# Kernel tuning notes

Measured on AMD Instinct MI355X. Metric: run time of the kernel, lower is better.

The kernel has to match this reference:

```python
import jax, jax.numpy as jnp
import numpy as np

B, W, K = 8, 200, 100   # batch, window_size, n_features
KS = 7                   # conv kernel size
HID = 150                # GRU hidden dim
ALPHA = 0.2              # leaky relu slope
FE = 2 * W               # feature GAT embed dim (gatv2 doubles window_size)
TE = 2 * K               # temporal GAT embed dim (gatv2 doubles n_features)


def setup_inputs() -> dict:
    key = jax.random.key(0)
    ks = jax.random.split(key, 16)
    s = lambda k, shape, sc=0.05: jax.random.normal(k, shape, jnp.float32) * sc
    return {
        "x": jax.random.normal(ks[0], (B, W, K), jnp.float32),
        "conv_w": s(ks[1], (K, K, KS)),
        "conv_b": s(ks[2], (K,)),
        "f_lin_w": s(ks[3], (2 * W, FE)),
        "f_lin_b": s(ks[4], (FE,)),
        "f_a": s(ks[5], (FE,)),
        "f_bias": s(ks[6], (K, K)),
        "t_lin_w": s(ks[7], (2 * K, TE)),
        "t_lin_b": s(ks[8], (TE,)),
        "t_a": s(ks[9], (TE,)),
        "t_bias": s(ks[10], (W, W)),
        "w_ih": s(ks[11], (3 * HID, 3 * K)),
        "w_hh": s(ks[12], (3 * HID, HID)),
        "b_ih": s(ks[13], (3 * HID,)),
        "b_hh": s(ks[14], (3 * HID,)),
    }


def _leaky(x):
    return jnp.where(x >= 0, x, ALPHA * x)


def _gatv2(v, lin_w, lin_b, a, bias):
    """GATv2 layer over fully-connected graph. v: (b, N, D).
    e_ij = a . leakyrelu(W [v_i || v_j] + b_lin); out = sigmoid(softmax(e+bias) @ v).
    Splitting W rows avoids materializing the (b,N,N,2D) concat tensor."""
    D = v.shape[-1]
    w1, w2 = lin_w[:D], lin_w[D:]
    si = jnp.einsum('bnd,de->bne', v, w1)  # contribution of node i (repeated)
    sj = jnp.einsum('bnd,de->bne', v, w2)  # contribution of node j (alternating)
    g = _leaky(si[:, :, None, :] + sj[:, None, :, :] + lin_b)  # (b,N,N,E)
    e = jnp.einsum('bije,e->bij', g, a) + bias                 # (b,N,N)
    attn = jax.nn.softmax(e, axis=2)
    return jax.nn.sigmoid(jnp.einsum('bij,bjd->bid', attn, v))  # (b,N,D)


def _forward(x, conv_w, conv_b, f_lin_w, f_lin_b, f_a, f_bias,
             t_lin_w, t_lin_b, t_a, t_bias, w_ih, w_hh, b_ih, b_hh):
    # ConvLayer: permute to (b,K,W), pad 3 both sides, conv1d k=7, relu, permute back
    xc = jnp.transpose(x, (0, 2, 1))
    xc = jax.lax.conv_general_dilated(xc, conv_w, (1,), [((KS - 1) // 2, (KS - 1) // 2)],
                                      dimension_numbers=('NCH', 'OIH', 'NCH'))
    xc = jax.nn.relu(xc + conv_b[None, :, None])
    xc = jnp.transpose(xc, (0, 2, 1))  # (b, W, K)

    # Feature GAT: nodes = features, per-node vector = window
    h_feat = _gatv2(jnp.transpose(xc, (0, 2, 1)), f_lin_w, f_lin_b, f_a, f_bias)
    h_feat = jnp.transpose(h_feat, (0, 2, 1))  # (b, W, K)
    # Temporal GAT: nodes = timesteps, per-node vector = features
    h_temp = _gatv2(xc, t_lin_w, t_lin_b, t_a, t_bias)  # (b, W, K)

    h_cat = jnp.concatenate([xc, h_feat, h_temp], axis=2)  # (b, W, 3K)

    # Single-layer GRU, torch gate order (r, z, n), batch_first; return final hidden
    def step(h, xt):
        gi = xt @ w_ih.T + b_ih
        gh = h @ w_hh.T + b_hh
        ir, iz, inn = jnp.split(gi, 3, axis=-1)
        hr, hz, hn = jnp.split(gh, 3, axis=-1)
        r = jax.nn.sigmoid(ir + hr)
        z = jax.nn.sigmoid(iz + hz)
        n = jnp.tanh(inn + r * hn)
        return (1.0 - z) * n + z * h, None

    h0 = jnp.zeros((x.shape[0], HID), x.dtype)
    h_end, _ = jax.lax.scan(step, h0, jnp.transpose(h_cat, (1, 0, 2)))
    return h_end  # (b, HID)


def reference(x, conv_w, conv_b, f_lin_w, f_lin_b, f_a, f_bias,
              t_lin_w, t_lin_b, t_a, t_bias, w_ih, w_hh, b_ih, b_hh):
    return _forward(x, conv_w, conv_b, f_lin_w, f_lin_b, f_a, f_bias,
                    t_lin_w, t_lin_b, t_a, t_bias, w_ih, w_hh, b_ih, b_hh)
```

## Files before the change

### kernel.cpp

```cpp
#include <hip/hip_runtime.h>
#include <math.h>

#define NB   8
#define NW   200
#define NK   100
#define KSZ  7
#define NHID 150
#define NFE  400
#define NTE  200
#define NG   450
#define NCIN 300
#define ALPHAC 0.2f

typedef __attribute__((ext_vector_type(8))) short bf8;
typedef __attribute__((ext_vector_type(4))) float f32x4;

__device__ __forceinline__ float sigmoidf_(float x){
  return 1.0f/(1.0f + __expf(-x));
}
__device__ __forceinline__ float tanhf_(float x){
  float xc = fminf(fmaxf(x, -15.f), 15.f);
  float e = __expf(2.f*xc);
  return (e - 1.f)/(e + 1.f);
}
__device__ __forceinline__ unsigned short f2bf(float f){
  unsigned int u = __float_as_uint(f);
  unsigned int r = u + 0x7FFFu + ((u>>16)&1u);
  return (unsigned short)(r>>16);
}

__global__ void prep_kernel(const float* conv_w, const float* w_ih, const float* w_hh,
                            float* conv_wT, float* w_ihT, unsigned int* Bfrag){
  int idx = blockIdx.x*256 + threadIdx.x;
  const int n1 = NK*NK*KSZ;
  const int n2 = NG*NCIN;
  const int n3 = 32*5*64*4;
  if (idx < n1){
    int k = idx % NK; int it = idx / NK;
    int i = it / KSZ, t = it % KSZ;
    conv_wT[idx] = conv_w[(k*NK + i)*KSZ + t];
  } else if (idx < n1 + n2){
    int o = idx - n1; int g = o % NG; int c = o / NG;
    w_ihT[o] = w_ih[g*NCIN + c];
  } else if (idx < n1 + n2 + n3){
    int o = idx - n1 - n2;
    int n   = o / 1280;
    int rem = o % 1280;
    int ks  = rem / 256;
    int rem2= rem % 256;
    int l   = rem2 >> 2;
    int d   = rem2 & 3;
    int col = n*16 + (l & 15);
    int k0  = ks*32 + (l >> 4)*8 + d*2;
    unsigned short lo = 0, hi = 0;
    if (col < NG){
      if (k0     < NHID) lo = f2bf(w_hh[col*NHID + k0]);
      if (k0 + 1 < NHID) hi = f2bf(w_hh[col*NHID + k0 + 1]);
    }
    Bfrag[o] = ((unsigned int)hi << 16) | lo;
  }
}

__global__ void conv_kernel(const float* x, const float* conv_b, const float* conv_wT, float* xc){
  int idx = blockIdx.x*256 + threadIdx.x;
  if (idx >= NB*NW*NK) return;
  int k = idx % NK; int w = (idx/NK) % NW; int b = idx/(NK*NW);
  float acc = conv_b[k];
  const float* xb = x + b*NW*NK;
  for (int t = 0; t < KSZ; ++t){
    int ws = w + t - 3;
    if (ws < 0 || ws >= NW) continue;
    const float* xr = xb + ws*NK;
    const float* wr = conv_wT + t*NK + k;
    #pragma unroll 4
    for (int i = 0; i < NK; ++i){
      acc += xr[i] * wr[i*KSZ*NK];
    }
  }
  xc[idx] = fmaxf(acc, 0.0f);
}

__global__ void fgat_sisj(const float* xc, const float* f_lin_w, float* si, float* sj){
  __shared__ __align__(16) float vt[NW*4];
  int b = blockIdx.x / 25; int n0 = (blockIdx.x % 25)*4;
  int tid = threadIdx.x;
  for (int idx = tid; idx < NW*4; idx += 512){
    int d = idx >> 2, nn = idx & 3;
    vt[idx] = xc[(b*NW + d)*NK + n0 + nn];
  }
  __syncthreads();
  if (tid >= NFE) return;
  int e = tid;
  float a1[4] = {0,0,0,0}, a2[4] = {0,0,0,0};
  for (int d = 0; d < NW; ++d){
    float w1 = f_lin_w[d*NFE + e];
    float w2 = f_lin_w[(NW + d)*NFE + e];
    float4 v = *(const float4*)&vt[d*4];
    a1[0] += v.x*w1; a1[1] += v.y*w1; a1[2] += v.z*w1; a1[3] += v.w*w1;
    a2[0] += v.x*w2; a2[1] += v.y*w2; a2[2] += v.z*w2; a2[3] += v.w*w2;
  }
  #pragma unroll
  for (int nn = 0; nn < 4; ++nn){
    si[(b*NK + n0+nn)*NFE + e] = a1[nn];
    sj[(b*NK + n0+nn)*NFE + e] = a2[nn];
  }
}

__global__ void tgat_sisj(const float* xc, const float* t_lin_w, float* si, float* sj){
  __shared__ __align__(16) float vt[NK*4];
  int b = blockIdx.x / 50; int n0 = (blockIdx.x % 50)*4;
  int tid = threadIdx.x;
  for (int idx = tid; idx < NK*4; idx += 256){
    int d = idx >> 2, nn = idx & 3;
    vt[idx] = xc[(b*NW + n0+nn)*NK + d];
  }
  __syncthreads();
  if (tid >= NTE) return;
  int e = tid;
  float a1[4] = {0,0,0,0}, a2[4] = {0,0,0,0};
  for (int d = 0; d < NK; ++d){
    float w1 = t_lin_w[d*NTE + e];
    float w2 = t_lin_w[(NK + d)*NTE + e];
    float4 v = *(const float4*)&vt[d*4];
    a1[0] += v.x*w1; a1[1] += v.y*w1; a1[2] += v.z*w1; a1[3] += v.w*w1;
    a2[0] += v.x*w2; a2[1] += v.y*w2; a2[2] += v.z*w2; a2[3] += v.w*w2;
  }
  #pragma unroll
  for (int nn = 0; nn < 4; ++nn){
    si[(b*NW + n0+nn)*NTE + e] = a1[nn];
    sj[(b*NW + n0+nn)*NTE + e] = a2[nn];
  }
}

__global__ void fgat_attn(const float* xc, const float* si, const float* sj,
                          const float* f_lin_b, const float* f_a, const float* f_bias,
                          float* h_featT){
  __shared__ float sib[NFE], av[NFE], attn[NK], red[128];
  int b = blockIdx.x / NK, i = blockIdx.x % NK;
  int tid = threadIdx.x;
  for (int e = tid; e < NFE; e += 128){
    sib[e] = si[(b*NK + i)*NFE + e] + f_lin_b[e];
    av[e]  = f_a[e];
  }
  __syncthreads();
  float ej = -1e30f;
  if (tid < NK){
    const float* sjr = sj + (b*NK + tid)*NFE;
    float acc = 0.f;
    for (int e = 0; e < NFE; ++e){
      float tv = sib[e] + sjr[e];
      float lk = fmaxf(tv, 0.f) + ALPHAC*fminf(tv, 0.f);
      acc += av[e]*lk;
    }
    ej = acc + f_bias[i*NK + tid];
  }
  red[tid] = ej; __syncthreads();
  for (int s = 64; s > 0; s >>= 1){ if (tid < s) red[tid] = fmaxf(red[tid], red[tid+s]); __syncthreads(); }
  float m = red[0]; __syncthreads();
  float ex = (tid < NK) ? __expf(ej - m) : 0.f;
  red[tid] = ex; __syncthreads();
  for (int s = 64; s > 0; s >>= 1){ if (tid < s) red[tid] += red[tid+s]; __syncthreads(); }
  float denom = red[0];
  if (tid < NK) attn[tid] = ex / denom;
  __syncthreads();
  for (int d = tid; d < NW; d += 128){
    const float* xr = xc + (b*NW + d)*NK;
    float acc = 0.f;
    for (int j = 0; j < NK; ++j) acc += attn[j]*xr[j];
    h_featT[(b*NW + d)*NK + i] = sigmoidf_(acc);
  }
}

__global__ void tgat_attn(const float* xc, const float* si, const float* sj,
                          const float* t_lin_b, const float* t_a, const float* t_bias,
                          float* h_temp){
  __shared__ float sib[NTE], av[NTE], attn[NW], red[256];
  int b = blockIdx.x / NW, i = blockIdx.x % NW;
  int tid = threadIdx.x;
  for (int e = tid; e < NTE; e += 256){
    sib[e] = si[(b*NW + i)*NTE + e] + t_lin_b[e];
    av[e]  = t_a[e];
  }
  __syncthreads();
  float ej = -1e30f;
  if (tid < NW){
    const float* sjr = sj + (b*NW + tid)*NTE;
    float acc = 0.f;
    for (int e = 0; e < NTE; ++e){
      float tv = sib[e] + sjr[e];
      float lk = fmaxf(tv, 0.f) + ALPHAC*fminf(tv, 0.f);
      acc += av[e]*lk;
    }
    ej = acc + t_bias[i*NW + tid];
  }
  red[tid] = ej; __syncthreads();
  for (int s = 128; s > 0; s >>= 1){ if (tid < s) red[tid] = fmaxf(red[tid], red[tid+s]); __syncthreads(); }
  float m = red[0]; __syncthreads();
  float ex = (tid < NW) ? __expf(ej - m) : 0.f;
  red[tid] = ex; __syncthreads();
  for (int s = 128; s > 0; s >>= 1){ if (tid < s) red[tid] += red[tid+s]; __syncthreads(); }
  float denom = red[0];
  if (tid < NW) attn[tid] = ex / denom;
  __syncthreads();
  for (int d = tid; d < NK; d += 256){
    float acc = 0.f;
    for (int j = 0; j < NW; ++j) acc += attn[j]*xc[(b*NW + j)*NK + d];
    h_temp[(b*NW + i)*NK + d] = sigmoidf_(acc);
  }
}

__global__ void gi_kernel(const float* xc, const float* h_featT, const float* h_temp,
                          const float* w_ihT, const float* b_ih, float* gi){
  __shared__ __align__(16) float hc[NCIN*8];
  int b = blockIdx.x / 25; int t0 = (blockIdx.x % 25)*8;
  int tid = threadIdx.x;
  for (int idx = tid; idx < NCIN*8; idx += 512){
    int tt = idx / NCIN; int c = idx % NCIN;
    int base = (b*NW + t0 + tt)*NK;
    float v;
    if (c < NK)        v = xc[base + c];
    else if (c < 2*NK) v = h_featT[base + c - NK];
    else               v = h_temp[base + c - 2*NK];
    hc[c*8 + tt] = v;
  }
  __syncthreads();
  if (tid >= NG) return;
  int g = tid;
  float bi = b_ih[g];
  float acc[8];
  #pragma unroll
  for (int tt = 0; tt < 8; ++tt) acc[tt] = bi;
  for (int c = 0; c < NCIN; ++c){
    float wv = w_ihT[c*NG + g];
    float4 h0 = *(const float4*)&hc[c*8];
    float4 h1 = *(const float4*)&hc[c*8+4];
    acc[0] += h0.x*wv; acc[1] += h0.y*wv; acc[2] += h0.z*wv; acc[3] += h0.w*wv;
    acc[4] += h1.x*wv; acc[5] += h1.y*wv; acc[6] += h1.z*wv; acc[7] += h1.w*wv;
  }
  #pragma unroll
  for (int tt = 0; tt < 8; ++tt)
    gi[((t0+tt)*NB + b)*NG + g] = acc[tt];
}

#define STASH(B0,B1,B2,B3, FR) { \
  int4 wq = Bq[(FR)*64 + lane]; \
  asm volatile("v_accvgpr_write_b32 " B0 ", %0\n\t" \
               "v_accvgpr_write_b32 " B1 ", %1\n\t" \
               "v_accvgpr_write_b32 " B2 ", %2\n\t" \
               "v_accvgpr_write_b32 " B3 ", %3" \
               :: "v"(wq.x), "v"(wq.y), "v"(wq.z), "v"(wq.w) \
               : B0, B1, B2, B3); }
#define MMA_INIT(ACC, AF, BR, C0,C1,C2,C3) \
  asm volatile("v_mfma_f32_16x16x32_bf16 %0, %1, " BR ", 0" \
               : "=v"(ACC) : "v"(AF) : C0,C1,C2,C3);
#define MMA_ACC(ACC, AF, BR, C0,C1,C2,C3) \
  asm volatile("v_mfma_f32_16x16x32_bf16 %0, %1, " BR ", %0" \
               : "+v"(ACC) : "v"(AF) : C0,C1,C2,C3);

__global__ void __launch_bounds__(512, 2) gru_kernel(const float* gi, const int4* Bq,
                                                     const float* b_hh, float* out){
  __shared__ __align__(16) unsigned short h_bf[16*176];
  __shared__ __align__(16) float h_f32[8*152];
  __shared__ __align__(16) float gh[16*516];
  int tid = threadIdx.x;
  int lane = tid & 63;
  int wv = tid >> 6;
  int agrp = lane >> 4;
  int arow = lane & 15;
  int crow = agrp*4;
  int ccol = arow;

  int p0 = tid, p1 = tid + 512, p2 = tid + 1024;
  int b0 = p0/NHID, u0 = p0%NHID;
  int b1 = p1/NHID, u1 = p1%NHID;
  bool v2 = (p2 < NB*NHID);
  int b2 = v2 ? p2/NHID : 0, u2 = v2 ? p2%NHID : 0;
  float bhr0 = b_hh[u0], bhz0 = b_hh[NHID+u0], bhn0 = b_hh[2*NHID+u0];
  float bhr1 = b_hh[u1], bhz1 = b_hh[NHID+u1], bhn1 = b_hh[2*NHID+u1];
  float bhr2 = b_hh[u2], bhz2 = b_hh[NHID+u2], bhn2 = b_hh[2*NHID+u2];

  STASH("a0","a1","a2","a3",     (wv)*5+0)
  STASH("a4","a5","a6","a7",     (wv)*5+1)
  STASH("a8","a9","a10","a11",   (wv)*5+2)
  STASH("a12","a13","a14","a15", (wv)*5+3)
  STASH("a16","a17","a18","a19", (wv)*5+4)
  STASH("a20","a21","a22","a23", (wv+8)*5+0)
  STASH("a24","a25","a26","a27", (wv+8)*5+1)
  STASH("a28","a29","a30","a31", (wv+8)*5+2)
  STASH("a32","a33","a34","a35", (wv+8)*5+3)
  STASH("a36","a37","a38","a39", (wv+8)*5+4)
  STASH("a40","a41","a42","a43", (wv+16)*5+0)
  STASH("a44","a45","a46","a47", (wv+16)*5+1)
  STASH("a48","a49","a50","a51", (wv+16)*5+2)
  STASH("a52","a53","a54","a55", (wv+16)*5+3)
  STASH("a56","a57","a58","a59", (wv+16)*5+4)
  STASH("a60","a61","a62","a63", (wv+24)*5+0)
  STASH("a64","a65","a66","a67", (wv+24)*5+1)
  STASH("a68","a69","a70","a71", (wv+24)*5+2)
  STASH("a72","a73","a74","a75", (wv+24)*5+3)
  STASH("a76","a77","a78","a79", (wv+24)*5+4)

  for (int i = tid; i < 16*176; i += 512) h_bf[i] = 0;
  for (int i = tid; i < 8*152;  i += 512) h_f32[i] = 0.f;
  __syncthreads();

  const bf8* HB = (const bf8*)h_bf;
  int abase = arow*22 + agrp;

  for (int t = 0; t < NW; ++t){
    const float* gt = gi + t*NB*NG;
    float gr0 = gt[b0*NG+u0], gz0 = gt[b0*NG+NHID+u0], gn0 = gt[b0*NG+2*NHID+u0];
    float gr1 = gt[b1*NG+u1], gz1 = gt[b1*NG+NHID+u1], gn1 = gt[b1*NG+2*NHID+u1];
    float gr2 = 0.f, gz2 = 0.f, gn2 = 0.f;
    if (v2){ gr2 = gt[b2*NG+u2]; gz2 = gt[b2*NG+NHID+u2]; gn2 = gt[b2*NG+2*NHID+u2]; }

    bf8 A0 = HB[abase],    A1 = HB[abase+4],  A2 = HB[abase+8],
        A3 = HB[abase+12], A4 = HB[abase+16];

    f32x4 c0, c1, c2, c3;
    MMA_INIT(c0, A0, "a[0:3]",   "a0","a1","a2","a3")
    MMA_INIT(c1, A0, "a[20:23]", "a20","a21","a22","a23")
    MMA_INIT(c2, A0, "a[40:43]", "a40","a41","a42","a43")
    MMA_INIT(c3, A0, "a[60:63]", "a60","a61","a62","a63")
    MMA_ACC (c0, A1, "a[4:7]",   "a4","a5","a6","a7")
    MMA_ACC (c1, A1, "a[24:27]", "a24","a25","a26","a27")
    MMA_ACC (c2, A1, "a[44:47]", "a44","a45","a46","a47")
    MMA_ACC (c3, A1, "a[64:67]", "a64","a65","a66","a67")
    MMA_ACC (c0, A2, "a[8:11]",  "a8","a9","a10","a11")
    MMA_ACC (c1, A2, "a[28:31]", "a28","a29","a30","a31")
    MMA_ACC (c2, A2, "a[48:51]", "a48","a49","a50","a51")
    MMA_ACC (c3, A2, "a[68:71]", "a68","a69","a70","a71")
    MMA_ACC (c0, A3, "a[12:15]", "a12","a13","a14","a15")
    MMA_ACC (c1, A3, "a[32:35]", "a32","a33","a34","a35")
    MMA_ACC (c2, A3, "a[52:55]", "a52","a53","a54","a55")
    MMA_ACC (c3, A3, "a[72:75]", "a72","a73","a74","a75")
    MMA_ACC (c0, A4, "a[16:19]", "a16","a17","a18","a19")
    MMA_ACC (c1, A4, "a[36:39]", "a36","a37","a38","a39")
    MMA_ACC (c2, A4, "a[56:59]", "a56","a57","a58","a59")
    MMA_ACC (c3, A4, "a[76:79]", "a76","a77","a78","a79")
    asm volatile("s_nop 7\n\ts_nop 7" ::: );

    {
      float* g0 = &gh[crow*516 + (wv   )*16 + ccol];
      float* g1 = &gh[crow*516 + (wv+ 8)*16 + ccol];
      float* g2 = &gh[crow*516 + (wv+16)*16 + ccol];
      float* g3 = &gh[crow*516 + (wv+24)*16 + ccol];
      g0[0]=c0[0]; g0[516]=c0[1]; g0[1032]=c0[2]; g0[1548]=c0[3];
      g1[0]=c1[0]; g1[516]=c1[1]; g1[1032]=c1[2]; g1[1548]=c1[3];
      g2[0]=c2[0]; g2[516]=c2[1]; g2[1032]=c2[2]; g2[1548]=c2[3];
      g3[0]=c3[0]; g3[516]=c3[1]; g3[1032]=c3[2]; g3[1548]=c3[3];
    }
    __syncthreads();

    {
      float r = sigmoidf_(gr0 + gh[b0*516+u0]        + gh[(8+b0)*516+u0]        + bhr0);
      float z = sigmoidf_(gz0 + gh[b0*516+NHID+u0]   + gh[(8+b0)*516+NHID+u0]   + bhz0);
      float n = tanhf_  (gn0 + r*(gh[b0*516+2*NHID+u0] + gh[(8+b0)*516+2*NHID+u0] + bhn0));
      float hold = h_f32[b0*152+u0];
      float hn = (1.f - z)*n + z*hold;
      h_f32[b0*152+u0] = hn;
      unsigned int ub = __float_as_uint(hn);
      unsigned int hi = (ub + 0x7FFFu + ((ub>>16)&1u)) >> 16;
      h_bf[b0*176+u0] = (unsigned short)hi;
      float lo = hn - __uint_as_float(hi<<16);
      unsigned int ul = __float_as_uint(lo);
      h_bf[(8+b0)*176+u0] = (unsigned short)((ul + 0x7FFFu + ((ul>>16)&1u)) >> 16);
    }
    {
      float r = sigmoidf_(gr1 + gh[b1*516+u1]        + gh[(8+b1)*516+u1]        + bhr1);
      float z = sigmoidf_(gz1 + gh[b1*516+NHID+u1]   + gh[(8+b1)*516+NHID+u1]   + bhz1);
      float n = tanhf_  (gn1 + r*(gh[b1*516+2*NHID+u1] + gh[(8+b1)*516+2*NHID+u1] + bhn1));
      float hold = h_f32[b1*152+u1];
      float hn = (1.f - z)*n + z*hold;
      h_f32[b1*152+u1] = hn;
      unsigned int ub = __float_as_uint(hn);
      unsigned int hi = (ub + 0x7FFFu + ((ub>>16)&1u)) >> 16;
      h_bf[b1*176+u1] = (unsigned short)hi;
      float lo = hn - __uint_as_float(hi<<16);
      unsigned int ul = __float_as_uint(lo);
      h_bf[(8+b1)*176+u1] = (unsigned short)((ul + 0x7FFFu + ((ul>>16)&1u)) >> 16);
    }
    if (v2){
      float r = sigmoidf_(gr2 + gh[b2*516+u2]        + gh[(8+b2)*516+u2]        + bhr2);
      float z = sigmoidf_(gz2 + gh[b2*516+NHID+u2]   + gh[(8+b2)*516+NHID+u2]   + bhz2);
      float n = tanhf_  (gn2 + r*(gh[b2*516+2*NHID+u2] + gh[(8+b2)*516+2*NHID+u2] + bhn2));
      float hold = h_f32[b2*152+u2];
      float hn = (1.f - z)*n + z*hold;
      h_f32[b2*152+u2] = hn;
      unsigned int ub = __float_as_uint(hn);
      unsigned int hi = (ub + 0x7FFFu + ((ub>>16)&1u)) >> 16;
      h_bf[b2*176+u2] = (unsigned short)hi;
      float lo = hn - __uint_as_float(hi<<16);
      unsigned int ul = __float_as_uint(lo);
      h_bf[(8+b2)*176+u2] = (unsigned short)((ul + 0x7FFFu + ((ul>>16)&1u)) >> 16);
    }
    __syncthreads();
  }

  out[b0*NHID + u0] = h_f32[b0*152 + u0];
  out[b1*NHID + u1] = h_f32[b1*152 + u1];
  if (v2) out[b2*NHID + u2] = h_f32[b2*152 + u2];
}

extern "C" void kernel_launch(void* const* d_in, const int* in_sizes, int n_in,
                              void* d_out, int out_size, void* d_ws, size_t ws_size,
                              hipStream_t stream){
  const float* x       = (const float*)d_in[0];
  const float* conv_w  = (const float*)d_in[1];
  const float* conv_b  = (const float*)d_in[2];
  const float* f_lin_w = (const float*)d_in[3];
  const float* f_lin_b = (const float*)d_in[4];
  const float* f_a     = (const float*)d_in[5];
  const float* f_bias  = (const float*)d_in[6];
  const float* t_lin_w = (const float*)d_in[7];
  const float* t_lin_b = (const float*)d_in[8];
  const float* t_a     = (const float*)d_in[9];
  const float* t_bias  = (const float*)d_in[10];
  const float* w_ih    = (const float*)d_in[11];
  const float* w_hh    = (const float*)d_in[12];
  const float* b_ih    = (const float*)d_in[13];
  const float* b_hh    = (const float*)d_in[14];

  float* ws      = (float*)d_ws;
  float* xc      = ws;
  float* conv_wT = ws + 160000;
  float* si_f    = ws + 230000;
  float* sj_f    = ws + 550000;
  float* h_featT = ws + 870000;
  float* si_t    = ws + 1030000;
  float* sj_t    = ws + 1350000;
  float* h_temp  = ws + 1670000;
  float* w_ihT   = ws + 1830000;
  float* gi      = ws + 1965000;
  float* BfragF  = ws + 2685000;

  prep_kernel<<<961, 256, 0, stream>>>(conv_w, w_ih, w_hh, conv_wT, w_ihT, (unsigned int*)BfragF);
  conv_kernel<<<(NB*NW*NK + 255)/256, 256, 0, stream>>>(x, conv_b, conv_wT, xc);
  fgat_sisj<<<NB*25, 512, 0, stream>>>(xc, f_lin_w, si_f, sj_f);
  tgat_sisj<<<NB*50, 256, 0, stream>>>(xc, t_lin_w, si_t, sj_t);
  fgat_attn<<<NB*NK, 128, 0, stream>>>(xc, si_f, sj_f, f_lin_b, f_a, f_bias, h_featT);
  tgat_attn<<<NB*NW, 256, 0, stream>>>(xc, si_t, sj_t, t_lin_b, t_a, t_bias, h_temp);
  gi_kernel<<<NB*25, 512, 0, stream>>>(xc, h_featT, h_temp, w_ihT, b_ih, gi);
  gru_kernel<<<1, 512, 0, stream>>>(gi, (const int4*)BfragF, b_hh, (float*)d_out);
}
```

Measured before the change: 434.7 us.

## Run GRU recurrence with 1024 threads, halving MFMA chains per wave

```diff
diff --git a/kernel.cpp b/kernel.cpp
--- a/kernel.cpp
+++ b/kernel.cpp
@@ -257,8 +257,8 @@
   asm volatile("v_mfma_f32_16x16x32_bf16 %0, %1, " BR ", %0" \
                : "+v"(ACC) : "v"(AF) : C0,C1,C2,C3);
 
-__global__ void __launch_bounds__(512, 2) gru_kernel(const float* gi, const int4* Bq,
-                                                     const float* b_hh, float* out){
+__global__ void __launch_bounds__(1024, 4) gru_kernel(const float* gi, const int4* Bq,
+                                                      const float* b_hh, float* out){
   __shared__ __align__(16) unsigned short h_bf[16*176];
   __shared__ __align__(16) float h_f32[8*152];
   __shared__ __align__(16) float gh[16*516];
@@ -270,38 +270,27 @@
   int crow = agrp*4;
   int ccol = arow;
 
-  int p0 = tid, p1 = tid + 512, p2 = tid + 1024;
+  int p0 = tid;
   int b0 = p0/NHID, u0 = p0%NHID;
-  int b1 = p1/NHID, u1 = p1%NHID;
-  bool v2 = (p2 < NB*NHID);
-  int b2 = v2 ? p2/NHID : 0, u2 = v2 ? p2%NHID : 0;
+  bool v1 = (tid < 176);
+  int p1 = tid + 1024;
+  int b1 = v1 ? p1/NHID : 0, u1 = v1 ? p1%NHID : 0;
   float bhr0 = b_hh[u0], bhz0 = b_hh[NHID+u0], bhn0 = b_hh[2*NHID+u0];
   float bhr1 = b_hh[u1], bhz1 = b_hh[NHID+u1], bhn1 = b_hh[2*NHID+u1];
-  float bhr2 = b_hh[u2], bhz2 = b_hh[NHID+u2], bhn2 = b_hh[2*NHID+u2];
 
   STASH("a0","a1","a2","a3",     (wv)*5+0)
   STASH("a4","a5","a6","a7",     (wv)*5+1)
   STASH("a8","a9","a10","a11",   (wv)*5+2)
   STASH("a12","a13","a14","a15", (wv)*5+3)
   STASH("a16","a17","a18","a19", (wv)*5+4)
-  STASH("a20","a21","a22","a23", (wv+8)*5+0)
-  STASH("a24","a25","a26","a27", (wv+8)*5+1)
-  STASH("a28","a29","a30","a31", (wv+8)*5+2)
-  STASH("a32","a33","a34","a35", (wv+8)*5+3)
-  STASH("a36","a37","a38","a39", (wv+8)*5+4)
-  STASH("a40","a41","a42","a43", (wv+16)*5+0)
-  STASH("a44","a45","a46","a47", (wv+16)*5+1)
-  STASH("a48","a49","a50","a51", (wv+16)*5+2)
-  STASH("a52","a53","a54","a55", (wv+16)*5+3)
-  STASH("a56","a57","a58","a59", (wv+16)*5+4)
-  STASH("a60","a61","a62","a63", (wv+24)*5+0)
-  STASH("a64","a65","a66","a67", (wv+24)*5+1)
-  STASH("a68","a69","a70","a71", (wv+24)*5+2)
-  STASH("a72","a73","a74","a75", (wv+24)*5+3)
-  STASH("a76","a77","a78","a79", (wv+24)*5+4)
-
-  for (int i = tid; i < 16*176; i += 512) h_bf[i] = 0;
-  for (int i = tid; i < 8*152;  i += 512) h_f32[i] = 0.f;
+  STASH("a20","a21","a22","a23", (wv+16)*5+0)
+  STASH("a24","a25","a26","a27", (wv+16)*5+1)
+  STASH("a28","a29","a30","a31", (wv+16)*5+2)
+  STASH("a32","a33","a34","a35", (wv+16)*5+3)
+  STASH("a36","a37","a38","a39", (wv+16)*5+4)
+
+  for (int i = tid; i < 16*176; i += 1024) h_bf[i] = 0;
+  for (int i = tid; i < 8*152;  i += 1024) h_f32[i] = 0.f;
   __syncthreads();
 
   const bf8* HB = (const bf8*)h_bf;
@@ -310,45 +299,30 @@
   for (int t = 0; t < NW; ++t){
     const float* gt = gi + t*NB*NG;
     float gr0 = gt[b0*NG+u0], gz0 = gt[b0*NG+NHID+u0], gn0 = gt[b0*NG+2*NHID+u0];
-    float gr1 = gt[b1*NG+u1], gz1 = gt[b1*NG+NHID+u1], gn1 = gt[b1*NG+2*NHID+u1];
-    float gr2 = 0.f, gz2 = 0.f, gn2 = 0.f;
-    if (v2){ gr2 = gt[b2*NG+u2]; gz2 = gt[b2*NG+NHID+u2]; gn2 = gt[b2*NG+2*NHID+u2]; }
+    float gr1 = 0.f, gz1 = 0.f, gn1 = 0.f;
+    if (v1){ gr1 = gt[b1*NG+u1]; gz1 = gt[b1*NG+NHID+u1]; gn1 = gt[b1*NG+2*NHID+u1]; }
 
     bf8 A0 = HB[abase],    A1 = HB[abase+4],  A2 = HB[abase+8],
         A3 = HB[abase+12], A4 = HB[abase+16];
 
-    f32x4 c0, c1, c2, c3;
+    f32x4 c0, c1;
     MMA_INIT(c0, A0, "a[0:3]",   "a0","a1","a2","a3")
     MMA_INIT(c1, A0, "a[20:23]", "a20","a21","a22","a23")
-    MMA_INIT(c2, A0, "a[40:43]", "a40","a41","a42","a43")
-    MMA_INIT(c3, A0, "a[60:63]", "a60","a61","a62","a63")
     MMA_ACC (c0, A1, "a[4:7]",   "a4","a5","a6","a7")
     MMA_ACC (c1, A1, "a[24:27]", "a24","a25","a26","a27")
-    MMA_ACC (c2, A1, "a[44:47]", "a44","a45","a46","a47")
-    MMA_ACC (c3, A1, "a[64:67]", "a64","a65","a66","a67")
     MMA_ACC (c0, A2, "a[8:11]",  "a8","a9","a10","a11")
     MMA_ACC (c1, A2, "a[28:31]", "a28","a29","a30","a31")
-    MMA_ACC (c2, A2, "a[48:51]", "a48","a49","a50","a51")
-    MMA_ACC (c3, A2, "a[68:71]", "a68","a69","a70","a71")
     MMA_ACC (c0, A3, "a[12:15]", "a12","a13","a14","a15")
     MMA_ACC (c1, A3, "a[32:35]", "a32","a33","a34","a35")
-    MMA_ACC (c2, A3, "a[52:55]", "a52","a53","a54","a55")
-    MMA_ACC (c3, A3, "a[72:75]", "a72","a73","a74","a75")
     MMA_ACC (c0, A4, "a[16:19]", "a16","a17","a18","a19")
     MMA_ACC (c1, A4, "a[36:39]", "a36","a37","a38","a39")
-    MMA_ACC (c2, A4, "a[56:59]", "a56","a57","a58","a59")
-    MMA_ACC (c3, A4, "a[76:79]", "a76","a77","a78","a79")
     asm volatile("s_nop 7\n\ts_nop 7" ::: );
 
     {
       float* g0 = &gh[crow*516 + (wv   )*16 + ccol];
-      float* g1 = &gh[crow*516 + (wv+ 8)*16 + ccol];
-      float* g2 = &gh[crow*516 + (wv+16)*16 + ccol];
-      float* g3 = &gh[crow*516 + (wv+24)*16 + ccol];
+      float* g1 = &gh[crow*516 + (wv+16)*16 + ccol];
       g0[0]=c0[0]; g0[516]=c0[1]; g0[1032]=c0[2]; g0[1548]=c0[3];
       g1[0]=c1[0]; g1[516]=c1[1]; g1[1032]=c1[2]; g1[1548]=c1[3];
-      g2[0]=c2[0]; g2[516]=c2[1]; g2[1032]=c2[2]; g2[1548]=c2[3];
-      g3[0]=c3[0]; g3[516]=c3[1]; g3[1032]=c3[2]; g3[1548]=c3[3];
     }
     __syncthreads();
 
@@ -366,7 +340,7 @@
       unsigned int ul = __float_as_uint(lo);
       h_bf[(8+b0)*176+u0] = (unsigned short)((ul + 0x7FFFu + ((ul>>16)&1u)) >> 16);
     }
-    {
+    if (v1){
       float r = sigmoidf_(gr1 + gh[b1*516+u1]        + gh[(8+b1)*516+u1]        + bhr1);
       float z = sigmoidf_(gz1 + gh[b1*516+NHID+u1]   + gh[(8+b1)*516+NHID+u1]   + bhz1);
       float n = tanhf_  (gn1 + r*(gh[b1*516+2*NHID+u1] + gh[(8+b1)*516+2*NHID+u1] + bhn1));
@@ -380,26 +354,11 @@
       unsigned int ul = __float_as_uint(lo);
       h_bf[(8+b1)*176+u1] = (unsigned short)((ul + 0x7FFFu + ((ul>>16)&1u)) >> 16);
     }
-    if (v2){
-      float r = sigmoidf_(gr2 + gh[b2*516+u2]        + gh[(8+b2)*516+u2]        + bhr2);
-      float z = sigmoidf_(gz2 + gh[b2*516+NHID+u2]   + gh[(8+b2)*516+NHID+u2]   + bhz2);
-      float n = tanhf_  (gn2 + r*(gh[b2*516+2*NHID+u2] + gh[(8+b2)*516+2*NHID+u2] + bhn2));
-      float hold = h_f32[b2*152+u2];
-      float hn = (1.f - z)*n + z*hold;
-      h_f32[b2*152+u2] = hn;
-      unsigned int ub = __float_as_uint(hn);
-      unsigned int hi = (ub + 0x7FFFu + ((ub>>16)&1u)) >> 16;
-      h_bf[b2*176+u2] = (unsigned short)hi;
-      float lo = hn - __uint_as_float(hi<<16);
-      unsigned int ul = __float_as_uint(lo);
-      h_bf[(8+b2)*176+u2] = (unsigned short)((ul + 0x7FFFu + ((ul>>16)&1u)) >> 16);
-    }
     __syncthreads();
   }
 
   out[b0*NHID + u0] = h_f32[b0*152 + u0];
-  out[b1*NHID + u1] = h_f32[b1*152 + u1];
-  if (v2) out[b2*NHID + u2] = h_f32[b2*152 + u2];
+  if (v1) out[b1*NHID + u1] = h_f32[b1*152 + u1];
 }
 
 extern "C" void kernel_launch(void* const* d_in, const int* in_sizes, int n_in,
@@ -441,5 +400,5 @@
   fgat_attn<<<NB*NK, 128, 0, stream>>>(xc, si_f, sj_f, f_lin_b, f_a, f_bias, h_featT);
   tgat_attn<<<NB*NW, 256, 0, stream>>>(xc, si_t, sj_t, t_lin_b, t_a, t_bias, h_temp);
   gi_kernel<<<NB*25, 512, 0, stream>>>(xc, h_featT, h_temp, w_ihT, b_ih, gi);
-  gru_kernel<<<1, 512, 0, stream>>>(gi, (const int4*)BfragF, b_hh, (float*)d_out);
-}
+  gru_kernel<<<1, 1024, 0, stream>>>(gi, (const int4*)BfragF, b_hh, (float*)d_out);
+}
```

After: 420.9 us. 1.03x faster.

## Restructure GRU step: 768 threads, prefetch gi, fold hi/lo partials, hidden in registers

Applied to the files above, without the earlier changes.

```diff
diff --git a/kernel.cpp b/kernel.cpp
--- a/kernel.cpp
+++ b/kernel.cpp
@@ -257,149 +257,144 @@
   asm volatile("v_mfma_f32_16x16x32_bf16 %0, %1, " BR ", %0" \
                : "+v"(ACC) : "v"(AF) : C0,C1,C2,C3);
 
-__global__ void __launch_bounds__(512, 2) gru_kernel(const float* gi, const int4* Bq,
-                                                     const float* b_hh, float* out){
-  __shared__ __align__(16) unsigned short h_bf[16*176];
-  __shared__ __align__(16) float h_f32[8*152];
-  __shared__ __align__(16) float gh[16*516];
+__global__ void __launch_bounds__(768) gru_kernel(const float* gi, const int4* Bq,
+                                                  const float* b_hh, float* out){
+  __shared__ __align__(16) unsigned short h_bf[16*184];
+  __shared__ __align__(16) float gh[512*10];
   int tid = threadIdx.x;
   int lane = tid & 63;
   int wv = tid >> 6;
   int agrp = lane >> 4;
   int arow = lane & 15;
-  int crow = agrp*4;
-  int ccol = arow;
-
-  int p0 = tid, p1 = tid + 512, p2 = tid + 1024;
-  int b0 = p0/NHID, u0 = p0%NHID;
-  int b1 = p1/NHID, u1 = p1%NHID;
-  bool v2 = (p2 < NB*NHID);
-  int b2 = v2 ? p2/NHID : 0, u2 = v2 ? p2%NHID : 0;
+
+  int b0 = tid/NHID, u0 = tid%NHID;
+  bool v1 = (tid < 432);
+  int p1 = tid + 768;
+  int b1 = v1 ? p1/NHID : 0, u1 = v1 ? p1%NHID : 0;
   float bhr0 = b_hh[u0], bhz0 = b_hh[NHID+u0], bhn0 = b_hh[2*NHID+u0];
   float bhr1 = b_hh[u1], bhz1 = b_hh[NHID+u1], bhn1 = b_hh[2*NHID+u1];
-  float bhr2 = b_hh[u2], bhz2 = b_hh[NHID+u2], bhn2 = b_hh[2*NHID+u2];
-
-  STASH("a0","a1","a2","a3",     (wv)*5+0)
-  STASH("a4","a5","a6","a7",     (wv)*5+1)
-  STASH("a8","a9","a10","a11",   (wv)*5+2)
-  STASH("a12","a13","a14","a15", (wv)*5+3)
-  STASH("a16","a17","a18","a19", (wv)*5+4)
-  STASH("a20","a21","a22","a23", (wv+8)*5+0)
-  STASH("a24","a25","a26","a27", (wv+8)*5+1)
-  STASH("a28","a29","a30","a31", (wv+8)*5+2)
-  STASH("a32","a33","a34","a35", (wv+8)*5+3)
-  STASH("a36","a37","a38","a39", (wv+8)*5+4)
-  STASH("a40","a41","a42","a43", (wv+16)*5+0)
-  STASH("a44","a45","a46","a47", (wv+16)*5+1)
-  STASH("a48","a49","a50","a51", (wv+16)*5+2)
-  STASH("a52","a53","a54","a55", (wv+16)*5+3)
-  STASH("a56","a57","a58","a59", (wv+16)*5+4)
-  STASH("a60","a61","a62","a63", (wv+24)*5+0)
-  STASH("a64","a65","a66","a67", (wv+24)*5+1)
-  STASH("a68","a69","a70","a71", (wv+24)*5+2)
-  STASH("a72","a73","a74","a75", (wv+24)*5+3)
-  STASH("a76","a77","a78","a79", (wv+24)*5+4)
-
-  for (int i = tid; i < 16*176; i += 512) h_bf[i] = 0;
-  for (int i = tid; i < 8*152;  i += 512) h_f32[i] = 0.f;
+
+  if (wv < 8){
+    STASH("a0","a1","a2","a3",     (wv)*5+0)
+    STASH("a4","a5","a6","a7",     (wv)*5+1)
+    STASH("a8","a9","a10","a11",   (wv)*5+2)
+    STASH("a12","a13","a14","a15", (wv)*5+3)
+    STASH("a16","a17","a18","a19", (wv)*5+4)
+    STASH("a20","a21","a22","a23", (wv+8)*5+0)
+    STASH("a24","a25","a26","a27", (wv+8)*5+1)
+    STASH("a28","a29","a30","a31", (wv+8)*5+2)
+    STASH("a32","a33","a34","a35", (wv+8)*5+3)
+    STASH("a36","a37","a38","a39", (wv+8)*5+4)
+    STASH("a40","a41","a42","a43", (wv+16)*5+0)
+    STASH("a44","a45","a46","a47", (wv+16)*5+1)
+    STASH("a48","a49","a50","a51", (wv+16)*5+2)
+    STASH("a52","a53","a54","a55", (wv+16)*5+3)
+    STASH("a56","a57","a58","a59", (wv+16)*5+4)
+    STASH("a60","a61","a62","a63", (wv+24)*5+0)
+    STASH("a64","a65","a66","a67", (wv+24)*5+1)
+    STASH("a68","a69","a70","a71", (wv+24)*5+2)
+    STASH("a72","a73","a74","a75", (wv+24)*5+3)
+    STASH("a76","a77","a78","a79", (wv+24)*5+4)
+  }
+
+  for (int i = tid; i < 16*184; i += 768) h_bf[i] = 0;
   __syncthreads();
 
   const bf8* HB = (const bf8*)h_bf;
-  int abase = arow*22 + agrp;
+  int abase = arow*23 + agrp;
+
+  float hold0 = 0.f, hold1 = 0.f;
+
+  float cr0, cz0, cn0, cr1 = 0.f, cz1 = 0.f, cn1 = 0.f;
+  {
+    const float* g0 = gi + b0*NG;
+    cr0 = g0[u0]; cz0 = g0[NHID+u0]; cn0 = g0[2*NHID+u0];
+    if (v1){
+      const float* g1 = gi + b1*NG;
+      cr1 = g1[u1]; cz1 = g1[NHID+u1]; cn1 = g1[2*NHID+u1];
+    }
+  }
 
   for (int t = 0; t < NW; ++t){
-    const float* gt = gi + t*NB*NG;
-    float gr0 = gt[b0*NG+u0], gz0 = gt[b0*NG+NHID+u0], gn0 = gt[b0*NG+2*NHID+u0];
-    float gr1 = gt[b1*NG+u1], gz1 = gt[b1*NG+NHID+u1], gn1 = gt[b1*NG+2*NHID+u1];
-    float gr2 = 0.f, gz2 = 0.f, gn2 = 0.f;
-    if (v2){ gr2 = gt[b2*NG+u2]; gz2 = gt[b2*NG+NHID+u2]; gn2 = gt[b2*NG+2*NHID+u2]; }
-
-    bf8 A0 = HB[abase],    A1 = HB[abase+4],  A2 = HB[abase+8],
-        A3 = HB[abase+12], A4 = HB[abase+16];
-
-    f32x4 c0, c1, c2, c3;
-    MMA_INIT(c0, A0, "a[0:3]",   "a0","a1","a2","a3")
-    MMA_INIT(c1, A0, "a[20:23]", "a20","a21","a22","a23")
-    MMA_INIT(c2, A0, "a[40:43]", "a40","a41","a42","a43")
-    MMA_INIT(c3, A0, "a[60:63]", "a60","a61","a62","a63")
-    MMA_ACC (c0, A1, "a[4:7]",   "a4","a5","a6","a7")
-    MMA_ACC (c1, A1, "a[24:27]", "a24","a25","a26","a27")
-    MMA_ACC (c2, A1, "a[44:47]", "a44","a45","a46","a47")
-    MMA_ACC (c3, A1, "a[64:67]", "a64","a65","a66","a67")
-    MMA_ACC (c0, A2, "a[8:11]",  "a8","a9","a10","a11")
-    MMA_ACC (c1, A2, "a[28:31]", "a28","a29","a30","a31")
-    MMA_ACC (c2, A2, "a[48:51]", "a48","a49","a50","a51")
-    MMA_ACC (c3, A2, "a[68:71]", "a68","a69","a70","a71")
-    MMA_ACC (c0, A3, "a[12:15]", "a12","a13","a14","a15")
-    MMA_ACC (c1, A3, "a[32:35]", "a32","a33","a34","a35")
-    MMA_ACC (c2, A3, "a[52:55]", "a52","a53","a54","a55")
-    MMA_ACC (c3, A3, "a[72:75]", "a72","a73","a74","a75")
-    MMA_ACC (c0, A4, "a[16:19]", "a16","a17","a18","a19")
-    MMA_ACC (c1, A4, "a[36:39]", "a36","a37","a38","a39")
-    MMA_ACC (c2, A4, "a[56:59]", "a56","a57","a58","a59")
-    MMA_ACC (c3, A4, "a[76:79]", "a76","a77","a78","a79")
-    asm volatile("s_nop 7\n\ts_nop 7" ::: );
+    int tn = (t+1 < NW) ? (t+1) : t;
+    const float* gt = gi + tn*NB*NG;
+    float nr0 = gt[b0*NG+u0], nz0 = gt[b0*NG+NHID+u0], nn0 = gt[b0*NG+2*NHID+u0];
+    float nr1 = 0.f, nz1 = 0.f, nn1 = 0.f;
+    if (v1){ nr1 = gt[b1*NG+u1]; nz1 = gt[b1*NG+NHID+u1]; nn1 = gt[b1*NG+2*NHID+u1]; }
+
+    if (wv < 8){
+      bf8 A0 = HB[abase],    A1 = HB[abase+4],  A2 = HB[abase+8],
+          A3 = HB[abase+12], A4 = HB[abase+16];
+      f32x4 c0, c1, c2, c3;
+      MMA_INIT(c0, A0, "a[0:3]",   "a0","a1","a2","a3")
+      MMA_INIT(c1, A0, "a[20:23]", "a20","a21","a22","a23")
+      MMA_INIT(c2, A0, "a[40:43]", "a40","a41","a42","a43")
+      MMA_INIT(c3, A0, "a[60:63]", "a60","a61","a62","a63")
+      MMA_ACC (c0, A1, "a[4:7]",   "a4","a5","a6","a7")
+      MMA_ACC (c1, A1, "a[24:27]", "a24","a25","a26","a27")
+      MMA_ACC (c2, A1, "a[44:47]", "a44","a45","a46","a47")
+      MMA_ACC (c3, A1, "a[64:67]", "a64","a65","a66","a67")
+      MMA_ACC (c0, A2, "a[8:11]",  "a8","a9","a10","a11")
+      MMA_ACC (c1, A2, "a[28:31]", "a28","a29","a30","a31")
+      MMA_ACC (c2, A2, "a[48:51]", "a48","a49","a50","a51")
+      MMA_ACC (c3, A2, "a[68:71]", "a68","a69","a70","a71")
+      MMA_ACC (c0, A3, "a[12:15]", "a12","a13","a14","a15")
+      MMA_ACC (c1, A3, "a[32:35]", "a32","a33","a34","a35")
+      MMA_ACC (c2, A3, "a[52:55]", "a52","a53","a54","a55")
+      MMA_ACC (c3, A3, "a[72:75]", "a72","a73","a74","a75")
+      MMA_ACC (c0, A4, "a[16:19]", "a16","a17","a18","a19")
+      MMA_ACC (c1, A4, "a[36:39]", "a36","a37","a38","a39")
+      MMA_ACC (c2, A4, "a[56:59]", "a56","a57","a58","a59")
+      MMA_ACC (c3, A4, "a[76:79]", "a76","a77","a78","a79")
+      asm volatile("s_nop 7\n\ts_nop 7" ::: );
+
+      int cb = agrp*2;
+      float2 s0, s1, s2, s3;
+      s0.x = c0[0]+c0[1]; s0.y = c0[2]+c0[3];
+      s1.x = c1[0]+c1[1]; s1.y = c1[2]+c1[3];
+      s2.x = c2[0]+c2[1]; s2.y = c2[2]+c2[3];
+      s3.x = c3[0]+c3[1]; s3.y = c3[2]+c3[3];
+      *(float2*)&gh[((wv    )*16 + arow)*10 + cb] = s0;
+      *(float2*)&gh[((wv+ 8)*16 + arow)*10 + cb] = s1;
+      *(float2*)&gh[((wv+16)*16 + arow)*10 + cb] = s2;
+      *(float2*)&gh[((wv+24)*16 + arow)*10 + cb] = s3;
+    }
+    __syncthreads();
 
     {
-      float* g0 = &gh[crow*516 + (wv   )*16 + ccol];
-      float* g1 = &gh[crow*516 + (wv+ 8)*16 + ccol];
-      float* g2 = &gh[crow*516 + (wv+16)*16 + ccol];
-      float* g3 = &gh[crow*516 + (wv+24)*16 + ccol];
-      g0[0]=c0[0]; g0[516]=c0[1]; g0[1032]=c0[2]; g0[1548]=c0[3];
-      g1[0]=c1[0]; g1[516]=c1[1]; g1[1032]=c1[2]; g1[1548]=c1[3];
-      g2[0]=c2[0]; g2[516]=c2[1]; g2[1032]=c2[2]; g2[1548]=c2[3];
-      g3[0]=c3[0]; g3[516]=c3[1]; g3[1032]=c3[2]; g3[1548]=c3[3];
-    }
-    __syncthreads();
-
-    {
-      float r = sigmoidf_(gr0 + gh[b0*516+u0]        + gh[(8+b0)*516+u0]        + bhr0);
-      float z = sigmoidf_(gz0 + gh[b0*516+NHID+u0]   + gh[(8+b0)*516+NHID+u0]   + bhz0);
-      float n = tanhf_  (gn0 + r*(gh[b0*516+2*NHID+u0] + gh[(8+b0)*516+2*NHID+u0] + bhn0));
-      float hold = h_f32[b0*152+u0];
-      float hn = (1.f - z)*n + z*hold;
-      h_f32[b0*152+u0] = hn;
+      float r = sigmoidf_(cr0 + gh[u0*10 + b0]        + bhr0);
+      float z = sigmoidf_(cz0 + gh[(NHID+u0)*10 + b0] + bhz0);
+      float n = tanhf_  (cn0 + r*(gh[(2*NHID+u0)*10 + b0] + bhn0));
+      float hn = (1.f - z)*n + z*hold0;
+      hold0 = hn;
       unsigned int ub = __float_as_uint(hn);
       unsigned int hi = (ub + 0x7FFFu + ((ub>>16)&1u)) >> 16;
-      h_bf[b0*176+u0] = (unsigned short)hi;
+      h_bf[(2*b0)*184 + u0] = (unsigned short)hi;
       float lo = hn - __uint_as_float(hi<<16);
       unsigned int ul = __float_as_uint(lo);
-      h_bf[(8+b0)*176+u0] = (unsigned short)((ul + 0x7FFFu + ((ul>>16)&1u)) >> 16);
-    }
-    {
-      float r = sigmoidf_(gr1 + gh[b1*516+u1]        + gh[(8+b1)*516+u1]        + bhr1);
-      float z = sigmoidf_(gz1 + gh[b1*516+NHID+u1]   + gh[(8+b1)*516+NHID+u1]   + bhz1);
-      float n = tanhf_  (gn1 + r*(gh[b1*516+2*NHID+u1] + gh[(8+b1)*516+2*NHID+u1] + bhn1));
-      float hold = h_f32[b1*152+u1];
-      float hn = (1.f - z)*n + z*hold;
-      h_f32[b1*152+u1] = hn;
+      h_bf[(2*b0+1)*184 + u0] = (unsigned short)((ul + 0x7FFFu + ((ul>>16)&1u)) >> 16);
+    }
+    if (v1){
+      float r = sigmoidf_(cr1 + gh[u1*10 + b1]        + bhr1);
+      float z = sigmoidf_(cz1 + gh[(NHID+u1)*10 + b1] + bhz1);
+      float n = tanhf_  (cn1 + r*(gh[(2*NHID+u1)*10 + b1] + bhn1));
+      float hn = (1.f - z)*n + z*hold1;
+      hold1 = hn;
       unsigned int ub = __float_as_uint(hn);
       unsigned int hi = (ub + 0x7FFFu + ((ub>>16)&1u)) >> 16;
-      h_bf[b1*176+u1] = (unsigned short)hi;
+      h_bf[(2*b1)*184 + u1] = (unsigned short)hi;
       float lo = hn - __uint_as_float(hi<<16);
       unsigned int ul = __float_as_uint(lo);
-      h_bf[(8+b1)*176+u1] = (unsigned short)((ul + 0x7FFFu + ((ul>>16)&1u)) >> 16);
-    }
-    if (v2){
-      float r = sigmoidf_(gr2 + gh[b2*516+u2]        + gh[(8+b2)*516+u2]        + bhr2);
-      float z = sigmoidf_(gz2 + gh[b2*516+NHID+u2]   + gh[(8+b2)*516+NHID+u2]   + bhz2);
-      float n = tanhf_  (gn2 + r*(gh[b2*516+2*NHID+u2] + gh[(8+b2)*516+2*NHID+u2] + bhn2));
-      float hold = h_f32[b2*152+u2];
-      float hn = (1.f - z)*n + z*hold;
-      h_f32[b2*152+u2] = hn;
-      unsigned int ub = __float_as_uint(hn);
-      unsigned int hi = (ub + 0x7FFFu + ((ub>>16)&1u)) >> 16;
-      h_bf[b2*176+u2] = (unsigned short)hi;
-      float lo = hn - __uint_as_float(hi<<16);
-      unsigned int ul = __float_as_uint(lo);
-      h_bf[(8+b2)*176+u2] = (unsigned short)((ul + 0x7FFFu + ((ul>>16)&1u)) >> 16);
+      h_bf[(2*b1+1)*184 + u1] = (unsigned short)((ul + 0x7FFFu + ((ul>>16)&1u)) >> 16);
     }
     __syncthreads();
-  }
-
-  out[b0*NHID + u0] = h_f32[b0*152 + u0];
-  out[b1*NHID + u1] = h_f32[b1*152 + u1];
-  if (v2) out[b2*NHID + u2] = h_f32[b2*152 + u2];
+
+    cr0 = nr0; cz0 = nz0; cn0 = nn0;
+    cr1 = nr1; cz1 = nz1; cn1 = nn1;
+  }
+
+  out[b0*NHID + u0] = hold0;
+  if (v1) out[b1*NHID + u1] = hold1;
 }
 
 extern "C" void kernel_launch(void* const* d_in, const int* in_sizes, int n_in,
@@ -441,5 +436,5 @@
   fgat_attn<<<NB*NK, 128, 0, stream>>>(xc, si_f, sj_f, f_lin_b, f_a, f_bias, h_featT);
   tgat_attn<<<NB*NW, 256, 0, stream>>>(xc, si_t, sj_t, t_lin_b, t_a, t_bias, h_temp);
   gi_kernel<<<NB*25, 512, 0, stream>>>(xc, h_featT, h_temp, w_ihT, b_ih, gi);
-  gru_kernel<<<1, 512, 0, stream>>>(gi, (const int4*)BfragF, b_hh, (float*)d_out);
-}
+  gru_kernel<<<1, 768, 0, stream>>>(gi, (const int4*)BfragF, b_hh, (float*)d_out);
+}
```

Result: faster. 409.5 us (-5.8%).
